# Performance work log

Measured on AMD Instinct MI355X. Metric: run time of the kernel, lower is better.

## Reference

```python
import jax, jax.numpy as jnp
import numpy as np

N = 10000      # atoms
F = 32         # nr_atom_basis
H = 7          # nr_heads
C = F * H      # nr_coefficients = 224
E = 200000     # edges
NRBF = 50
CUTOFF = 5.0
EPS = 1e-8


def _seg_sum(x, idx, n):
    return jax.ops.segment_sum(x, idx, num_segments=n)


def _seg_mean(x, idx, n):
    # torch scatter_reduce 'mean' with include_self=False: sum/count, 0 for empty segments
    s = _seg_sum(x, idx, n)
    cnt = _seg_sum(jnp.ones((x.shape[0],), x.dtype), idx, n)
    cnt = jnp.maximum(cnt, 1.0).reshape((n,) + (1,) * (x.ndim - 1))
    return s / cnt


def _scatter_softmax(w, idx, n):
    m = jax.ops.segment_max(w, idx, num_segments=n)
    m = jnp.where(jnp.isfinite(m), m, 0.0)  # guard empty segments
    e = jnp.exp(w - m[idx])
    s = _seg_sum(e, idx, n)
    return e / s[idx]


def setup_inputs():
    key = jax.random.key(0)
    ks = jax.random.split(key, 16)
    def w(k, shape, scale=0.1):
        return jax.random.normal(k, shape, jnp.float32) * scale
    return {
        "h": w(ks[0], (N, F), 1.0),
        "x": w(ks[1], (N, 3), 1.0),
        "v": w(ks[2], (N, 3), 0.1),
        "pairlist": jax.random.randint(ks[3], (2, E), 0, N),
        "w_in": w(ks[4], (2 * F, NRBF)), "b_in": jnp.zeros((NRBF,), jnp.float32),
        "w_e1": w(ks[5], (2 * F + NRBF + 1, F)), "b_e1": jnp.zeros((F,), jnp.float32),
        "w_e2": w(ks[6], (F, F)), "b_e2": jnp.zeros((F,), jnp.float32),
        "w_att": w(ks[7], (F, H)), "b_att": jnp.zeros((H,), jnp.float32),
        "w_n1": w(ks[8], (F + C + F, F)), "b_n1": jnp.zeros((F,), jnp.float32),
        "w_n2": w(ks[9], (F, F)), "b_n2": jnp.zeros((F,), jnp.float32),
        "w_pn1": w(ks[10], (C, F)), "b_pn1": jnp.zeros((F,), jnp.float32),
        "w_pn2": w(ks[11], (F, F)), "b_pn2": jnp.zeros((F,), jnp.float32),
        "w_v1": w(ks[12], (F, F)), "b_v1": jnp.zeros((F,), jnp.float32),
        "w_v2": w(ks[13], (F, 1)),
        "w_xmix": w(ks[14], (C, C)),
        "w_vmix": w(ks[15], (C, 1)),
    }


def reference(h, x, v, pairlist, w_in, b_in, w_e1, b_e1, w_e2, b_e2,
              w_att, b_att, w_n1, b_n1, w_n2, b_n2, w_pn1, b_pn1,
              w_pn2, b_pn2, w_v1, b_v1, w_v2, w_xmix, w_vmix):
    act = jax.nn.silu
    idx_i, idx_j = pairlist[0], pairlist[1]
    n = h.shape[0]

    r_ij = x[idx_j] - x[idx_i]                      # [E,3]
    d_ij = jnp.linalg.norm(r_ij, axis=-1)           # [E]
    dir_ij = r_ij / (d_ij[:, None] + EPS)           # [E,3]

    # edge model: continuous-filter conv with concatenation
    h_cat = jnp.concatenate([h[idx_i], h[idx_j]], axis=-1)           # [E,2F]
    centers = jnp.linspace(0.0, CUTOFF, NRBF)
    width = centers[1] - centers[0]
    rbf = jnp.exp(-0.5 * ((d_ij[:, None] - centers) / width) ** 2)   # [E,NRBF]
    filt = rbf * (h_cat @ w_in + b_in)                               # [E,NRBF]
    edge_in = jnp.concatenate([h_cat, filt, d_ij[:, None]], axis=-1)
    h_ij_edge = act(edge_in @ w_e1 + b_e1) @ w_e2 + b_e2             # [E,F]

    # semantic attention (scatter softmax over edges grouped by idx_i)
    att_w = jax.nn.celu(h_ij_edge @ w_att + b_att, alpha=2.0)        # [E,H]
    cut = 0.5 * (jnp.cos(jnp.pi * d_ij / CUTOFF) + 1.0) * (d_ij < CUTOFF)
    att = _scatter_softmax(att_w * cut[:, None], idx_i, n)           # [E,H]
    # einsum('pf,ph->pfh').reshape -> f-major, h-minor
    h_ij_sem = (h_ij_edge[:, :, None] * att[:, None, :]).reshape(-1, C)  # [E,C]
    h_i_sem = _seg_sum(h_ij_sem, idx_i, n)                           # [N,C]

    # equivariant combinations + spatial attention
    comb = jnp.tanh(h_ij_sem @ w_xmix)[:, :, None] * dir_ij[:, None, :]  # [E,C,3]
    comb_mean = _seg_mean(comb, idx_i, n)                            # [N,C,3]
    cnsq = jnp.sum(comb_mean ** 2, axis=-1)                          # [N,C]
    h_i_spatial = act(act(cnsq @ w_pn1 + b_pn1) @ w_pn2 + b_pn2)     # [N,F]

    # node update
    node_in = jnp.concatenate([h, h_i_sem, h_i_spatial], axis=-1)
    h_upd = h + act(act(node_in @ w_n1 + b_n1) @ w_n2 + b_n2)        # [N,F]

    # velocity update
    v_ij = jnp.einsum('ecx,c->ex', comb, w_vmix[:, 0])               # [E,3]
    dv = _seg_mean(v_ij, idx_i, n)                                   # [N,3]
    gate = 2.0 * jax.nn.sigmoid(act(h @ w_v1 + b_v1) @ w_v2)         # [N,1]
    v_upd = gate * v + dv
    x_upd = x + v_upd
    return h_upd, x_upd, v_upd
```

## Files before the change

kernel.cpp:

```cpp
#include <hip/hip_runtime.h>
#include <hip/hip_bf16.h>
#include <math.h>

typedef unsigned short u16;
typedef __attribute__((ext_vector_type(8))) short bf16x8;
typedef __attribute__((ext_vector_type(4))) float f32x4;

constexpr int kF    = 32;
constexpr int kH    = 7;
constexpr int kC    = 224;
constexpr int kRBF  = 50;
constexpr int kM    = 128;
constexpr int kStr  = 232;
constexpr int kEM   = 128;
constexpr int kAStr = 136;
constexpr int kBStr = 40;
constexpr float kCut = 5.0f;
constexpr float kEps = 1e-8f;

__device__ __forceinline__ float silu_f(float a) { return a / (1.f + __expf(-a)); }
__device__ __forceinline__ float tanh_f(float x) {
    float e = __expf(2.f * x);
    return 1.f - 2.f / (e + 1.f);
}
__device__ __forceinline__ float bf2f(u16 u) {
    union { unsigned int i; float f; } v; v.i = ((unsigned int)u) << 16; return v.f;
}
__device__ __forceinline__ u16 f2bf(float f) {
    union { float f; unsigned int i; } v; v.f = f;
    unsigned int x = v.i;
    unsigned int round = ((x >> 16) & 1u) + 0x7fffu;
    return (u16)((x + round) >> 16);
}
__device__ __forceinline__ unsigned pk2(float a, float b) {
    union { __hip_bfloat162 h; unsigned u; } v;
    v.h = __float22bfloat162_rn(make_float2(a, b));
    return v.u;
}

__global__ __launch_bounds__(256) void init_kernel(
    const float* __restrict__ wx, const float* __restrict__ w_in,
    const float* __restrict__ w_e1, const float* __restrict__ w_e2,
    const float* __restrict__ w_att, const float* __restrict__ b_e2,
    const float* __restrict__ b_att, const int* __restrict__ pl,
    u16* __restrict__ wxT, u16* __restrict__ W1T, u16* __restrict__ W2T,
    u16* __restrict__ W3T, u16* __restrict__ W24T, float* __restrict__ b24,
    int* __restrict__ counts, int E_)
{
    int idx = blockIdx.x * 256 + threadIdx.x;
    if (idx < kC * kC) {
        int c = idx / kC, k = idx - c * kC;
        wxT[idx] = f2bf(wx[k * kC + c]);
    }
    for (int e = idx; e < E_; e += gridDim.x * 256) atomicAdd(&counts[pl[e]], 1);

    if (blockIdx.x == 0) {
        int t = threadIdx.x;
        for (int i = t; i < 64 * 64; i += 256) {
            int n = i >> 6, k = i & 63;
            W1T[i] = f2bf((n < kRBF) ? w_in[k * kRBF + n] : 0.f);
        }
        for (int i = t; i < 32 * 128; i += 256) {
            int n = i >> 7, k = i & 127;
            W2T[i] = f2bf((k < 115) ? w_e1[k * kF + n] : 0.f);
        }
        for (int i = t; i < 32 * 32; i += 256) {
            int n = i >> 5, k = i & 31;
            W3T[i] = f2bf(w_e2[k * kF + n]);
        }
        for (int i = t; i < 16 * 32; i += 256) {
            int n = i >> 5, k = i & 31;
            float a = 0.f;
            if (n < kH) for (int o = 0; o < kF; o++) a += w_e2[k * kF + o] * w_att[o * kH + n];
            W24T[i] = f2bf(a);
        }
        if (t < kH) {
            float a = b_att[t];
            for (int o = 0; o < kF; o++) a += b_e2[o] * w_att[o * kH + t];
            b24[t] = a;
        }
    }
}

__global__ __launch_bounds__(1024) void scan_kernel(
    const int* __restrict__ counts, int* __restrict__ offsets, int n)
{
    __shared__ int buf[1024];
    int t = threadIdx.x;
    int chunk = (n + 1023) >> 10;
    int lo = t * chunk;
    int s = 0;
    for (int i = 0; i < chunk; i++) {
        int g = lo + i;
        if (g < n) s += counts[g];
    }
    buf[t] = s;
    __syncthreads();
    for (int off = 1; off < 1024; off <<= 1) {
        int v = (t >= off) ? buf[t - off] : 0;
        __syncthreads();
        buf[t] += v;
        __syncthreads();
    }
    int run = buf[t] - s;
    for (int i = 0; i < chunk; i++) {
        int g = lo + i;
        if (g < n) { offsets[g] = run; run += counts[g]; }
    }
    if (t == 1023) offsets[n] = buf[1023];
}

__global__ __launch_bounds__(256) void scatter_kernel(
    const int* __restrict__ pl, const int* __restrict__ offsets,
    int* __restrict__ cursor, int* __restrict__ rank, int* __restrict__ nid, int E_)
{
    int e = blockIdx.x * 256 + threadIdx.x;
    if (e < E_) {
        int i = pl[e];
        int p = atomicAdd(&cursor[i], 1);
        int pos = offsets[i] + p;
        rank[e] = pos;
        nid[pos] = i;
    }
}

__global__ __launch_bounds__(256) void edge_kernel(
    const float* __restrict__ h, const float* __restrict__ x,
    const int* __restrict__ pl, const int* __restrict__ rank_g, int E_,
    const float* __restrict__ b_in, const float* __restrict__ b_e1,
    const float* __restrict__ b_e2,
    const u16* __restrict__ W1T, const u16* __restrict__ W2T,
    const u16* __restrict__ W3T, const u16* __restrict__ W24T,
    const float* __restrict__ b24,
    float* __restrict__ he_g, float* __restrict__ logit_g,
    float* __restrict__ dir_g)
{
    __shared__ __align__(16) u16 s_A[kEM][kAStr];
    __shared__ __align__(16) u16 s_t1[kEM][kBStr];
    __shared__ float s_d[kEM];
    __shared__ int   s_r[kEM];

    int t = threadIdx.x;
    int T0 = blockIdx.x * kEM;
    int w = t >> 6, lane = t & 63, quad = lane >> 4, l15 = lane & 15;

    {
        int e = t >> 1, half = t & 1;
        int ge = T0 + e;
        bool val = ge < E_;
        int i = 0, j = 0;
        if (val) { i = pl[ge]; j = pl[E_ + ge]; }
        const float4* pi = (const float4*)(h + (size_t)i * kF) + half * 4;
        const float4* pj = (const float4*)(h + (size_t)j * kF) + half * 4;
#pragma unroll
        for (int q = 0; q < 4; q++) {
            float4 a = val ? pi[q] : make_float4(0.f, 0.f, 0.f, 0.f);
            float4 b = val ? pj[q] : make_float4(0.f, 0.f, 0.f, 0.f);
            unsigned* di = (unsigned*)&s_A[e][half * 16 + 4 * q];
            di[0] = pk2(a.x, a.y); di[1] = pk2(a.z, a.w);
            unsigned* dj = (unsigned*)&s_A[e][kF + half * 16 + 4 * q];
            dj[0] = pk2(b.x, b.y); dj[1] = pk2(b.z, b.w);
        }
        if (half == 0) {
            float d = 0.f;
            int r = 0;
            if (val) {
                r = rank_g[ge];
                float r0 = x[j * 3 + 0] - x[i * 3 + 0];
                float r1 = x[j * 3 + 1] - x[i * 3 + 1];
                float r2 = x[j * 3 + 2] - x[i * 3 + 2];
                d = sqrtf(r0 * r0 + r1 * r1 + r2 * r2);
                float inv = 1.0f / (d + kEps);
                dir_g[(size_t)r * 3 + 0] = r0 * inv;
                dir_g[(size_t)r * 3 + 1] = r1 * inv;
                dir_g[(size_t)r * 3 + 2] = r2 * inv;
            }
            s_r[e] = r;
            s_d[e] = d;
            s_A[e][114] = f2bf(d);
            s_A[e][115] = 0;
            unsigned* z = (unsigned*)&s_A[e][116];
#pragma unroll
            for (int q = 0; q < 6; q++) z[q] = 0u;
        }
    }
    __syncthreads();

    const float invw = 49.0f / kCut;

    {
        bf16x8 a1[2][2];
#pragma unroll
        for (int rt = 0; rt < 2; rt++)
#pragma unroll
            for (int kt = 0; kt < 2; kt++)
                a1[rt][kt] = *(const bf16x8*)&s_A[32 * w + 16 * rt + l15][kt * 32 + quad * 8];
#pragma unroll
        for (int ct = 0; ct < 4; ct++) {
            int c = ct * 16 + l15;
            bf16x8 b0 = *(const bf16x8*)(W1T + (size_t)c * 64 + quad * 8);
            bf16x8 b1 = *(const bf16x8*)(W1T + (size_t)c * 64 + 32 + quad * 8);
            float bin = (c < kRBF) ? b_in[c] : 0.f;
#pragma unroll
            for (int rt = 0; rt < 2; rt++) {
                f32x4 acc = {0.f, 0.f, 0.f, 0.f};
                acc = __builtin_amdgcn_mfma_f32_16x16x32_bf16(a1[rt][0], b0, acc, 0, 0, 0);
                acc = __builtin_amdgcn_mfma_f32_16x16x32_bf16(a1[rt][1], b1, acc, 0, 0, 0);
                if (c < kRBF) {
#pragma unroll
                    for (int r = 0; r < 4; r++) {
                        int row = 32 * w + 16 * rt + quad * 4 + r;
                        float arg = s_d[row] * invw - (float)c;
                        float filt = __expf(-0.5f * arg * arg) * (acc[r] + bin);
                        s_A[row][64 + c] = f2bf(filt);
                    }
                }
            }
        }
    }

    {
        bf16x8 a2[2][4];
#pragma unroll
        for (int rt = 0; rt < 2; rt++)
#pragma unroll
            for (int kt = 0; kt < 4; kt++)
                a2[rt][kt] = *(const bf16x8*)&s_A[32 * w + 16 * rt + l15][kt * 32 + quad * 8];
#pragma unroll
        for (int ct = 0; ct < 2; ct++) {
            int c = ct * 16 + l15;
            bf16x8 bb[4];
#pragma unroll
            for (int kt = 0; kt < 4; kt++)
                bb[kt] = *(const bf16x8*)(W2T + (size_t)c * 128 + kt * 32 + quad * 8);
            float be = b_e1[c];
#pragma unroll
            for (int rt = 0; rt < 2; rt++) {
                f32x4 acc = {0.f, 0.f, 0.f, 0.f};
#pragma unroll
                for (int kt = 0; kt < 4; kt++)
                    acc = __builtin_amdgcn_mfma_f32_16x16x32_bf16(a2[rt][kt], bb[kt], acc, 0, 0, 0);
#pragma unroll
                for (int r = 0; r < 4; r++) {
                    int row = 32 * w + 16 * rt + quad * 4 + r;
                    s_t1[row][c] = f2bf(silu_f(acc[r] + be));
                }
            }
        }
    }

    {
        bf16x8 a3[2];
#pragma unroll
        for (int rt = 0; rt < 2; rt++)
            a3[rt] = *(const bf16x8*)&s_t1[32 * w + 16 * rt + l15][quad * 8];

#pragma unroll
        for (int ct = 0; ct < 2; ct++) {
            int c = ct * 16 + l15;
            bf16x8 b3 = *(const bf16x8*)(W3T + (size_t)c * 32 + quad * 8);
            float be = b_e2[c];
#pragma unroll
            for (int rt = 0; rt < 2; rt++) {
                f32x4 acc = {0.f, 0.f, 0.f, 0.f};
                acc = __builtin_amdgcn_mfma_f32_16x16x32_bf16(a3[rt], b3, acc, 0, 0, 0);
#pragma unroll
                for (int r = 0; r < 4; r++) {
                    int row = 32 * w + 16 * rt + quad * 4 + r;
                    int ge = T0 + row;
                    if (ge < E_) he_g[(size_t)s_r[row] * kF + c] = acc[r] + be;
                }
            }
        }
        {
            bf16x8 b4 = *(const bf16x8*)(W24T + (size_t)l15 * 32 + quad * 8);
            float bb = (l15 < kH) ? b24[l15] : 0.f;
#pragma unroll
            for (int rt = 0; rt < 2; rt++) {
                f32x4 acc = {0.f, 0.f, 0.f, 0.f};
                acc = __builtin_amdgcn_mfma_f32_16x16x32_bf16(a3[rt], b4, acc, 0, 0, 0);
                if (l15 < kH) {
#pragma unroll
                    for (int r = 0; r < 4; r++) {
                        int row = 32 * w + 16 * rt + quad * 4 + r;
                        int ge = T0 + row;
                        if (ge < E_) {
                            float a = acc[r] + bb;
                            a = (a >= 0.f) ? a : 2.f * (__expf(0.5f * a) - 1.f);
                            float dd = s_d[row];
                            float cut = (dd < kCut)
                                ? 0.5f * (__cosf(0.62831853071795864f * dd) + 1.f) : 0.f;
                            logit_g[(size_t)s_r[row] * kH + l15] = a * cut;
                        }
                    }
                }
            }
        }
    }
}

__global__ __launch_bounds__(256) void stats_kernel(
    const float* __restrict__ logit_g, const int* __restrict__ offsets,
    float* __restrict__ m_g, float* __restrict__ invs_g, int N_)
{
    int wave = threadIdx.x >> 6;
    int lane = threadIdx.x & 63;
    int node = blockIdx.x * 4 + wave;
    if (node >= N_) return;
    int base = offsets[node];
    int deg  = offsets[node + 1] - base;

    float m[kH], ss[kH];
#pragma unroll
    for (int hh = 0; hh < kH; hh++) { m[hh] = -1e30f; ss[hh] = 0.f; }
    for (int e = lane; e < deg; e += 64) {
        const float* lp = logit_g + (size_t)(base + e) * kH;
#pragma unroll
        for (int hh = 0; hh < kH; hh++) {
            float vv = lp[hh];
            if (vv > m[hh]) { ss[hh] *= __expf(m[hh] - vv); m[hh] = vv; }
            ss[hh] += __expf(vv - m[hh]);
        }
    }
#pragma unroll
    for (int hh = 0; hh < kH; hh++) {
        float mm = m[hh], s2 = ss[hh];
#pragma unroll
        for (int off = 32; off >= 1; off >>= 1) {
            float mo = __shfl_xor(mm, off);
            float so = __shfl_xor(s2, off);
            float mn = fmaxf(mm, mo);
            s2 = s2 * __expf(mm - mn) + so * __expf(mo - mn);
            mm = mn;
        }
        if (lane == 0) {
            m_g[(size_t)node * kH + hh] = mm;
            invs_g[(size_t)node * kH + hh] = (s2 > 0.f) ? 1.f / s2 : 0.f;
        }
    }
}

__global__ __launch_bounds__(256) void xmix_kernel(
    const float* __restrict__ he_g, const float* __restrict__ logit_g,
    const float* __restrict__ dir_g, const int* __restrict__ nid,
    const float* __restrict__ m_g, const float* __restrict__ invs_g,
    const u16* __restrict__ wxT, int E_,
    float* __restrict__ nodeacc, float* __restrict__ bpart, int* __restrict__ bid)
{
    __shared__ __align__(16) u16 s_buf[kM][kStr];
    __shared__ float s_att[kM][kH];
    __shared__ __align__(16) float s_dir4[kM][4];
    __shared__ int   s_node[kM];
    __shared__ int   s_prev, s_next;

    int t = threadIdx.x;
    int T0 = blockIdx.x * kM;
    int cp = min(kM, E_ - T0);

    if (t < kM) s_node[t] = (T0 + t < E_) ? nid[T0 + t] : -1;
    if (t == 0) {
        s_prev = (T0 > 0) ? nid[T0 - 1] : -2;
        s_next = (T0 + cp < E_) ? nid[T0 + cp] : -2;
    }
    __syncthreads();

    int w    = t >> 6;
    int lane = t & 63;
    int quad = lane >> 4;
    int l15  = lane & 15;

    int ws = 32 * w;
    int we = min(ws + 32, cp);
    bool winvalid = (ws < cp);
    bool contL = false, contR = false;
    if (winvalid) {
        int nfirst = s_node[ws], nlast = s_node[we - 1];
        contL = (w == 0) ? (s_prev == nfirst) : (s_node[ws - 1] == nfirst);
        contR = (we == cp) ? (s_next == nlast) : (s_node[we] == nlast);
    }
    if (lane == 0) {
        int b0 = -1, b1 = -1;
        if (winvalid) {
            int nfirst = s_node[ws], nlast = s_node[we - 1];
            b0 = contL ? nfirst : -1;
            if (contR && !(nfirst == nlast && contL)) b1 = nlast;
        }
        bid[8 * blockIdx.x + 2 * w + 0] = b0;
        bid[8 * blockIdx.x + 2 * w + 1] = b1;
    }
    bool active_w = winvalid && (lane < 56);
    int c0 = 4 * lane;

    for (int idx = t; idx < kM * kH; idx += 256) {
        int e = idx / kH, hh = idx - e * kH;
        float a = 0.f;
        if (T0 + e < E_) {
            int nd = s_node[e];
            a = __expf(logit_g[(size_t)(T0 + e) * kH + hh] - m_g[(size_t)nd * kH + hh])
                * invs_g[(size_t)nd * kH + hh];
        }
        s_att[e][hh] = a;
    }
    for (int idx = t; idx < cp * 3; idx += 256) {
        int e = idx / 3, xx = idx - e * 3;
        s_dir4[e][xx] = dir_g[(size_t)(T0 + e) * 3 + xx];
    }
    __syncthreads();

#pragma unroll
    for (int p = 0; p < kM * kF / 256; p++) {
        int idx = t + 256 * p;
        int e = idx >> 5, f = idx & 31;
        float hv = (T0 + e < E_) ? he_g[(size_t)(T0 + e) * kF + f] : 0.f;
        float sv[7];
#pragma unroll
        for (int hh = 0; hh < kH; hh++) sv[hh] = hv * s_att[e][hh];
        u16* dst = &s_buf[e][f * 7];
        if ((f & 1) == 0) {
            *(unsigned*)(dst)     = pk2(sv[0], sv[1]);
            *(unsigned*)(dst + 2) = pk2(sv[2], sv[3]);
            *(unsigned*)(dst + 4) = pk2(sv[4], sv[5]);
            dst[6] = f2bf(sv[6]);
        } else {
            dst[0] = f2bf(sv[0]);
            *(unsigned*)(dst + 1) = pk2(sv[1], sv[2]);
            *(unsigned*)(dst + 3) = pk2(sv[3], sv[4]);
            *(unsigned*)(dst + 5) = pk2(sv[5], sv[6]);
        }
    }
    __syncthreads();

    if (active_w) {
        float hs0 = 0.f, hs1 = 0.f, hs2 = 0.f, hs3 = 0.f;
        int rs = ws;
        for (int e = ws; e < we; e++) {
            if (s_node[e] != s_node[rs]) {
                bool comp = (rs > ws) || !contL;
                float4 vv = make_float4(hs0, hs1, hs2, hs3);
                if (comp) *(float4*)&nodeacc[(size_t)s_node[rs] * 896 + 672 + c0] = vv;
                else *(float4*)&bpart[(size_t)(8 * blockIdx.x + 2 * w) * 896 + 672 + c0] = vv;
                hs0 = hs1 = hs2 = hs3 = 0.f; rs = e;
            }
            uint2 pv = *(const uint2*)&s_buf[e][c0];
            hs0 += bf2f((u16)pv.x); hs1 += bf2f((u16)(pv.x >> 16));
            hs2 += bf2f((u16)pv.y); hs3 += bf2f((u16)(pv.y >> 16));
        }
        bool t0 = (rs == ws);
        bool comp = ((!t0) || !contL) && !contR;
        float4 vv = make_float4(hs0, hs1, hs2, hs3);
        if (comp) *(float4*)&nodeacc[(size_t)s_node[rs] * 896 + 672 + c0] = vv;
        else {
            int slot = (t0 && contL) ? 0 : 1;
            *(float4*)&bpart[(size_t)(8 * blockIdx.x + 2 * w + slot) * 896 + 672 + c0] = vv;
        }
    }

    bf16x8 afr[2][7];
#pragma unroll
    for (int rt = 0; rt < 2; rt++)
#pragma unroll
        for (int kt = 0; kt < 7; kt++)
            afr[rt][kt] = *(const bf16x8*)&s_buf[32 * w + 16 * rt + l15][kt * 32 + quad * 8];

    bf16x8 bb[3][7];
#pragma unroll
    for (int kt = 0; kt < 7; kt++)
        bb[0][kt] = *(const bf16x8*)(wxT + (size_t)l15 * kC + kt * 32 + quad * 8);
#pragma unroll
    for (int kt = 0; kt < 7; kt++)
        bb[1][kt] = *(const bf16x8*)(wxT + (size_t)(16 + l15) * kC + kt * 32 + quad * 8);
    __syncthreads();

#pragma unroll
    for (int ct = 0; ct < 14; ct++) {
        const int cur = ct % 3;
        const int nxt = (ct + 2) % 3;
        if (ct < 12) {
            const u16* bp = wxT + (size_t)((ct + 2) * 16 + l15) * kC + quad * 8;
#pragma unroll
            for (int kt = 0; kt < 7; kt++) bb[nxt][kt] = *(const bf16x8*)(bp + kt * 32);
        }
        f32x4 acc0 = {0.f, 0.f, 0.f, 0.f};
        f32x4 acc1 = {0.f, 0.f, 0.f, 0.f};
#pragma unroll
        for (int kt = 0; kt < 7; kt++) {
            acc0 = __builtin_amdgcn_mfma_f32_16x16x32_bf16(afr[0][kt], bb[cur][kt], acc0, 0, 0, 0);
            acc1 = __builtin_amdgcn_mfma_f32_16x16x32_bf16(afr[1][kt], bb[cur][kt], acc1, 0, 0, 0);
        }
        int colg = ct * 16 + l15;
#pragma unroll
        for (int s = 0; s < 2; s++) {
            f32x4 ac = s ? acc1 : acc0;
            int rbase = 32 * w + 16 * s + quad * 4;
            unsigned p01 = pk2(tanh_f(ac[0]), tanh_f(ac[1]));
            unsigned p23 = pk2(tanh_f(ac[2]), tanh_f(ac[3]));
            s_buf[rbase + 0][colg] = (u16)p01;
            s_buf[rbase + 1][colg] = (u16)(p01 >> 16);
            s_buf[rbase + 2][colg] = (u16)p23;
            s_buf[rbase + 3][colg] = (u16)(p23 >> 16);
        }
    }
    __syncthreads();

    if (active_w) {
        float a0[4] = {0.f, 0.f, 0.f, 0.f};
        float a1[4] = {0.f, 0.f, 0.f, 0.f};
        float a2[4] = {0.f, 0.f, 0.f, 0.f};
        int rs = ws;
        for (int e = ws; e < we; e++) {
            if (s_node[e] != s_node[rs]) {
                bool comp = (rs > ws) || !contL;
                float* p = comp ? (nodeacc + (size_t)s_node[rs] * 896)
                                : (bpart + (size_t)(8 * blockIdx.x + 2 * w) * 896);
                *(float4*)&p[c0]       = make_float4(a0[0], a0[1], a0[2], a0[3]);
                *(float4*)&p[224 + c0] = make_float4(a1[0], a1[1], a1[2], a1[3]);
                *(float4*)&p[448 + c0] = make_float4(a2[0], a2[1], a2[2], a2[3]);
#pragma unroll
                for (int q = 0; q < 4; q++) { a0[q] = 0.f; a1[q] = 0.f; a2[q] = 0.f; }
                rs = e;
            }
            float4 dd = *(const float4*)&s_dir4[e][0];
            uint2 pv = *(const uint2*)&s_buf[e][c0];
            float Tv[4];
            Tv[0] = bf2f((u16)pv.x); Tv[1] = bf2f((u16)(pv.x >> 16));
            Tv[2] = bf2f((u16)pv.y); Tv[3] = bf2f((u16)(pv.y >> 16));
#pragma unroll
            for (int q = 0; q < 4; q++) {
                a0[q] += Tv[q] * dd.x;
                a1[q] += Tv[q] * dd.y;
                a2[q] += Tv[q] * dd.z;
            }
        }
        bool t0 = (rs == ws);
        bool comp = ((!t0) || !contL) && !contR;
        float* p;
        if (comp) p = nodeacc + (size_t)s_node[rs] * 896;
        else {
            int slot = (t0 && contL) ? 0 : 1;
            p = bpart + (size_t)(8 * blockIdx.x + 2 * w + slot) * 896;
        }
        *(float4*)&p[c0]       = make_float4(a0[0], a0[1], a0[2], a0[3]);
        *(float4*)&p[224 + c0] = make_float4(a1[0], a1[1], a1[2], a1[3]);
        *(float4*)&p[448 + c0] = make_float4(a2[0], a2[1], a2[2], a2[3]);
    }
}

__global__ __launch_bounds__(256) void node_kernel(
    const float* __restrict__ h, const float* __restrict__ x, const float* __restrict__ v,
    const float* __restrict__ nodeacc, const float* __restrict__ bpart,
    const int* __restrict__ bid, const int* __restrict__ offs,
    const float* __restrict__ w_n1, const float* __restrict__ b_n1,
    const float* __restrict__ w_n2, const float* __restrict__ b_n2,
    const float* __restrict__ w_pn1, const float* __restrict__ b_pn1,
    const float* __restrict__ w_pn2, const float* __restrict__ b_pn2,
    const float* __restrict__ w_v1, const float* __restrict__ b_v1,
    const float* __restrict__ w_v2, const float* __restrict__ w_vmix,
    float* __restrict__ out_h, float* __restrict__ out_x, float* __restrict__ out_v,
    int N_)
{
    __shared__ float s_cm[4][3][kC];
    __shared__ float s_cnsq[4][kC];
    __shared__ float s_ni[4][288];
    __shared__ float s_part[8][4][kF];
    __shared__ float s_hn[4][kF], s_sp1[4][kF], s_spat[4][kF], s_n1v[4][kF], s_g1[4][kF];
    __shared__ float s_pdv[4][3][8];
    __shared__ float s_gate[4], s_dv[4][3];

    int t = threadIdx.x;
    int n0 = blockIdx.x * 4;

    if (t < kC) {
        for (int nd = 0; nd < 4; nd++) {
            int node = n0 + nd;
            if (node >= N_) break;
            int base = offs[node], end = offs[node + 1];
            int deg = end - base;
            float a0 = 0.f, a1 = 0.f, a2 = 0.f, hh = 0.f;
            if (deg > 0) {
                int wlo = base >> 5, whi = (end - 1) >> 5;
                if (wlo == whi) {
                    const float* p = nodeacc + (size_t)node * 896;
                    a0 = p[t]; a1 = p[224 + t]; a2 = p[448 + t]; hh = p[672 + t];
                } else {
                    for (int W = wlo; W <= whi; W++) {
#pragma unroll
                        for (int s = 0; s < 2; s++) {
                            if (bid[2 * W + s] == node) {
                                const float* p = bpart + (size_t)(2 * W + s) * 896;
                                a0 += p[t]; a1 += p[224 + t]; a2 += p[448 + t]; hh += p[672 + t];
                            }
                        }
                    }
                }
            }
            float invc = 1.f / fmaxf((float)deg, 1.f);
            float m0 = a0 * invc, m1 = a1 * invc, m2 = a2 * invc;
            s_cm[nd][0][t] = m0; s_cm[nd][1][t] = m1; s_cm[nd][2][t] = m2;
            s_cnsq[nd][t] = m0 * m0 + m1 * m1 + m2 * m2;
            s_ni[nd][kF + t] = hh;
        }
    } else {
        int ln = t - 224;
        for (int nd = 0; nd < 4; nd++) {
            int node = n0 + nd;
            float hv = (node < N_) ? h[(size_t)node * kF + ln] : 0.f;
            s_hn[nd][ln] = hv;
            s_ni[nd][ln] = hv;
        }
    }
    __syncthreads();

    int o = t & 31, g = t >> 5;
    {
        float acc[4] = {0.f, 0.f, 0.f, 0.f};
        int cb = g * 28;
        for (int i = 0; i < 28; i++) {
            float wv = w_pn1[(cb + i) * kF + o];
#pragma unroll
            for (int nd = 0; nd < 4; nd++) acc[nd] += s_cnsq[nd][cb + i] * wv;
        }
#pragma unroll
        for (int nd = 0; nd < 4; nd++) s_part[g][nd][o] = acc[nd];
    }
    __syncthreads();
    if (t < 128) {
        int nd = t >> 5;
        float a = b_pn1[o];
#pragma unroll
        for (int g2 = 0; g2 < 8; g2++) a += s_part[g2][nd][o];
        s_sp1[nd][o] = silu_f(a);
    } else {
        int nd = (t - 128) >> 5;
        float a = b_v1[o];
        for (int f = 0; f < kF; f++) a += s_hn[nd][f] * w_v1[f * kF + o];
        s_g1[nd][o] = silu_f(a);
    }
    __syncthreads();
    if (t < 128) {
        int nd = t >> 5;
        float a = b_pn2[o];
        for (int o2 = 0; o2 < kF; o2++) a += s_sp1[nd][o2] * w_pn2[o2 * kF + o];
        s_spat[nd][o] = silu_f(a);
    } else if (t < 132) {
        int nd = t - 128;
        float a = 0.f;
        for (int o2 = 0; o2 < kF; o2++) a += s_g1[nd][o2] * w_v2[o2];
        s_gate[nd] = 2.f / (1.f + __expf(-a));
    } else if (t >= 160) {
        int q = t - 160; int nd = q / 24; int r = q - nd * 24;
        int xx = r >> 3, ln = r & 7;
        float a = 0.f;
        for (int c = ln; c < kC; c += 8) a += w_vmix[c] * s_cm[nd][xx][c];
        s_pdv[nd][xx][ln] = a;
    }
    __syncthreads();
    if (t < 128) {
        int nd = t >> 5;
        s_ni[nd][kF + kC + o] = s_spat[nd][o];
    } else if (t < 140) {
        int q = t - 128; int nd = q / 3; int xx = q - nd * 3;
        float a = 0.f;
#pragma unroll
        for (int ln = 0; ln < 8; ln++) a += s_pdv[nd][xx][ln];
        s_dv[nd][xx] = a;
    }
    __syncthreads();
    {
        float acc[4] = {0.f, 0.f, 0.f, 0.f};
        int rb = g * 36;
        for (int i = 0; i < 36; i++) {
            float wv = w_n1[(rb + i) * kF + o];
#pragma unroll
            for (int nd = 0; nd < 4; nd++) acc[nd] += s_ni[nd][rb + i] * wv;
        }
#pragma unroll
        for (int nd = 0; nd < 4; nd++) s_part[g][nd][o] = acc[nd];
    }
    __syncthreads();
    if (t < 128) {
        int nd = t >> 5;
        float a = b_n1[o];
#pragma unroll
        for (int g2 = 0; g2 < 8; g2++) a += s_part[g2][nd][o];
        s_n1v[nd][o] = silu_f(a);
    }
    __syncthreads();
    if (t < 128) {
        int nd = t >> 5; int node = n0 + nd;
        if (node < N_) {
            float a = b_n2[o];
            for (int o2 = 0; o2 < kF; o2++) a += s_n1v[nd][o2] * w_n2[o2 * kF + o];
            out_h[(size_t)node * kF + o] = s_hn[nd][o] + silu_f(a);
        }
    } else if (t < 140) {
        int q = t - 128; int nd = q / 3; int xx = q - nd * 3;
        int node = n0 + nd;
        if (node < N_) {
            float vv = v[(size_t)node * 3 + xx];
            float vu = s_gate[nd] * vv + s_dv[nd][xx];
            out_v[(size_t)node * 3 + xx] = vu;
            out_x[(size_t)node * 3 + xx] = x[(size_t)node * 3 + xx] + vu;
        }
    }
}

extern "C" void kernel_launch(void* const* d_in, const int* in_sizes, int n_in,
                              void* d_out, int out_size, void* d_ws, size_t ws_size,
                              hipStream_t stream)
{
    const float* h      = (const float*)d_in[0];
    const float* x      = (const float*)d_in[1];
    const float* v      = (const float*)d_in[2];
    const int*   pl     = (const int*)d_in[3];
    const float* w_in   = (const float*)d_in[4];
    const float* b_in   = (const float*)d_in[5];
    const float* w_e1   = (const float*)d_in[6];
    const float* b_e1   = (const float*)d_in[7];
    const float* w_e2   = (const float*)d_in[8];
    const float* b_e2   = (const float*)d_in[9];
    const float* w_att  = (const float*)d_in[10];
    const float* b_att  = (const float*)d_in[11];
    const float* w_n1   = (const float*)d_in[12];
    const float* b_n1   = (const float*)d_in[13];
    const float* w_n2   = (const float*)d_in[14];
    const float* b_n2   = (const float*)d_in[15];
    const float* w_pn1  = (const float*)d_in[16];
    const float* b_pn1  = (const float*)d_in[17];
    const float* w_pn2  = (const float*)d_in[18];
    const float* b_pn2  = (const float*)d_in[19];
    const float* w_v1   = (const float*)d_in[20];
    const float* b_v1   = (const float*)d_in[21];
    const float* w_v2   = (const float*)d_in[22];
    const float* w_xmix = (const float*)d_in[23];
    const float* w_vmix = (const float*)d_in[24];

    const int E_ = in_sizes[3] / 2;
    const int N_ = in_sizes[0] / kF;
    const int nblk = (E_ + kM - 1) / kM;

    char* w = (char*)d_ws;
    u16*   wxT     = (u16*)w;   w += (size_t)kC * kC * 2;
    u16*   W1T     = (u16*)w;   w += (size_t)64 * 64 * 2;
    u16*   W2T     = (u16*)w;   w += (size_t)32 * 128 * 2;
    u16*   W3T     = (u16*)w;   w += (size_t)32 * 32 * 2;
    u16*   W24T    = (u16*)w;   w += (size_t)16 * 32 * 2;
    float* b24     = (float*)w; w += 8 * 4;
    float* he_g    = (float*)w; w += (size_t)E_ * kF * 4;
    float* logit_g = (float*)w; w += (size_t)E_ * kH * 4;
    float* dir_g   = (float*)w; w += (size_t)E_ * 3 * 4;
    float* m_g     = (float*)w; w += (size_t)N_ * kH * 4;
    float* invs_g  = (float*)w; w += (size_t)N_ * kH * 4;
    float* nodeacc = (float*)w; w += (size_t)N_ * 896 * 4;
    float* bpart   = (float*)w; w += (size_t)8 * nblk * 896 * 4;
    int*   bid     = (int*)w;   w += (size_t)8 * nblk * 4;
    int* counts    = (int*)w;   w += (size_t)N_ * 4;
    int* offs      = (int*)w;   w += (size_t)(N_ + 1) * 4;
    int* cursor    = (int*)w;   w += (size_t)N_ * 4;
    int* rank_g    = (int*)w;   w += (size_t)E_ * 4;
    int* nid       = (int*)w;   w += (size_t)E_ * 4;

    float* out_h = (float*)d_out;
    float* out_x = out_h + (size_t)N_ * kF;
    float* out_v = out_x + (size_t)N_ * 3;

    hipMemsetAsync(counts, 0, (size_t)N_ * 4, stream);
    hipMemsetAsync(cursor, 0, (size_t)N_ * 4, stream);

    init_kernel<<<dim3((kC * kC + 255) / 256), dim3(256), 0, stream>>>(
        w_xmix, w_in, w_e1, w_e2, w_att, b_e2, b_att, pl,
        wxT, W1T, W2T, W3T, W24T, b24, counts, E_);

    scan_kernel<<<dim3(1), dim3(1024), 0, stream>>>(counts, offs, N_);

    scatter_kernel<<<dim3((E_ + 255) / 256), dim3(256), 0, stream>>>(
        pl, offs, cursor, rank_g, nid, E_);

    edge_kernel<<<dim3((E_ + kEM - 1) / kEM), dim3(256), 0, stream>>>(
        h, x, pl, rank_g, E_, b_in, b_e1, b_e2, W1T, W2T, W3T, W24T, b24,
        he_g, logit_g, dir_g);

    stats_kernel<<<dim3((N_ + 3) / 4), dim3(256), 0, stream>>>(
        logit_g, offs, m_g, invs_g, N_);

    xmix_kernel<<<dim3(nblk), dim3(256), 0, stream>>>(
        he_g, logit_g, dir_g, nid, m_g, invs_g, wxT, E_,
        nodeacc, bpart, bid);

    node_kernel<<<dim3((N_ + 3) / 4), dim3(256), 0, stream>>>(
        h, x, v, nodeacc, bpart, bid, offs,
        w_n1, b_n1, w_n2, b_n2, w_pn1, b_pn1, w_pn2, b_pn2,
        w_v1, b_v1, w_v2, w_vmix, out_h, out_x, out_v, N_);
}
```

Measured before the change: 348.4 us.

## Fuse scatter into edge kernel, store edge features as bf16, retune stats and prefetch

Drops the separate scatter kernel: the edge kernel now claims each edge's CSR slot with an atomic on the cursor and writes nid itself, which removes one launch and the rank array round trip. Per-edge hidden features are stored as bf16 rather than fp32, halving that intermediate's traffic at some precision cost. The stats kernel moves from one 64-lane wave per node to a 32-lane group per node, since degrees are around 20. The xmix weight prefetch goes from 3 to 4 buffers, which raises register pressure.

```diff
diff --git a/kernel.cpp b/kernel.cpp
--- a/kernel.cpp
+++ b/kernel.cpp
@@ -110,29 +110,16 @@
     if (t == 1023) offsets[n] = buf[1023];
 }
 
-__global__ __launch_bounds__(256) void scatter_kernel(
-    const int* __restrict__ pl, const int* __restrict__ offsets,
-    int* __restrict__ cursor, int* __restrict__ rank, int* __restrict__ nid, int E_)
-{
-    int e = blockIdx.x * 256 + threadIdx.x;
-    if (e < E_) {
-        int i = pl[e];
-        int p = atomicAdd(&cursor[i], 1);
-        int pos = offsets[i] + p;
-        rank[e] = pos;
-        nid[pos] = i;
-    }
-}
-
 __global__ __launch_bounds__(256) void edge_kernel(
     const float* __restrict__ h, const float* __restrict__ x,
-    const int* __restrict__ pl, const int* __restrict__ rank_g, int E_,
+    const int* __restrict__ pl, const int* __restrict__ offs,
+    int* __restrict__ cursor, int* __restrict__ nid, int E_,
     const float* __restrict__ b_in, const float* __restrict__ b_e1,
     const float* __restrict__ b_e2,
     const u16* __restrict__ W1T, const u16* __restrict__ W2T,
     const u16* __restrict__ W3T, const u16* __restrict__ W24T,
     const float* __restrict__ b24,
-    float* __restrict__ he_g, float* __restrict__ logit_g,
+    u16* __restrict__ he_g, float* __restrict__ logit_g,
     float* __restrict__ dir_g)
 {
     __shared__ __align__(16) u16 s_A[kEM][kAStr];
@@ -165,7 +152,9 @@
             float d = 0.f;
             int r = 0;
             if (val) {
-                r = rank_g[ge];
+                int p = atomicAdd(&cursor[i], 1);
+                r = offs[i] + p;
+                nid[r] = i;
                 float r0 = x[j * 3 + 0] - x[i * 3 + 0];
                 float r1 = x[j * 3 + 1] - x[i * 3 + 1];
                 float r2 = x[j * 3 + 2] - x[i * 3 + 2];
@@ -268,7 +257,7 @@
                 for (int r = 0; r < 4; r++) {
                     int row = 32 * w + 16 * rt + quad * 4 + r;
                     int ge = T0 + row;
-                    if (ge < E_) he_g[(size_t)s_r[row] * kF + c] = acc[r] + be;
+                    if (ge < E_) he_g[(size_t)s_r[row] * kF + c] = f2bf(acc[r] + be);
                 }
             }
         }
@@ -303,9 +292,9 @@
     const float* __restrict__ logit_g, const int* __restrict__ offsets,
     float* __restrict__ m_g, float* __restrict__ invs_g, int N_)
 {
-    int wave = threadIdx.x >> 6;
-    int lane = threadIdx.x & 63;
-    int node = blockIdx.x * 4 + wave;
+    int grp  = threadIdx.x >> 5;
+    int lane = threadIdx.x & 31;
+    int node = blockIdx.x * 8 + grp;
     if (node >= N_) return;
     int base = offsets[node];
     int deg  = offsets[node + 1] - base;
@@ -313,7 +302,7 @@
     float m[kH], ss[kH];
 #pragma unroll
     for (int hh = 0; hh < kH; hh++) { m[hh] = -1e30f; ss[hh] = 0.f; }
-    for (int e = lane; e < deg; e += 64) {
+    for (int e = lane; e < deg; e += 32) {
         const float* lp = logit_g + (size_t)(base + e) * kH;
 #pragma unroll
         for (int hh = 0; hh < kH; hh++) {
@@ -326,7 +315,7 @@
     for (int hh = 0; hh < kH; hh++) {
         float mm = m[hh], s2 = ss[hh];
 #pragma unroll
-        for (int off = 32; off >= 1; off >>= 1) {
+        for (int off = 16; off >= 1; off >>= 1) {
             float mo = __shfl_xor(mm, off);
             float so = __shfl_xor(s2, off);
             float mn = fmaxf(mm, mo);
@@ -341,7 +330,7 @@
 }
 
 __global__ __launch_bounds__(256) void xmix_kernel(
-    const float* __restrict__ he_g, const float* __restrict__ logit_g,
+    const u16* __restrict__ he_g, const float* __restrict__ logit_g,
     const float* __restrict__ dir_g, const int* __restrict__ nid,
     const float* __restrict__ m_g, const float* __restrict__ invs_g,
     const u16* __restrict__ wxT, int E_,
@@ -411,7 +400,7 @@
     for (int p = 0; p < kM * kF / 256; p++) {
         int idx = t + 256 * p;
         int e = idx >> 5, f = idx & 31;
-        float hv = (T0 + e < E_) ? he_g[(size_t)(T0 + e) * kF + f] : 0.f;
+        float hv = (T0 + e < E_) ? bf2f(he_g[(size_t)(T0 + e) * kF + f]) : 0.f;
         float sv[7];
 #pragma unroll
         for (int hh = 0; hh < kH; hh++) sv[hh] = hv * s_att[e][hh];
@@ -462,21 +451,20 @@
         for (int kt = 0; kt < 7; kt++)
             afr[rt][kt] = *(const bf16x8*)&s_buf[32 * w + 16 * rt + l15][kt * 32 + quad * 8];
 
-    bf16x8 bb[3][7];
-#pragma unroll
-    for (int kt = 0; kt < 7; kt++)
-        bb[0][kt] = *(const bf16x8*)(wxT + (size_t)l15 * kC + kt * 32 + quad * 8);
-#pragma unroll
-    for (int kt = 0; kt < 7; kt++)
-        bb[1][kt] = *(const bf16x8*)(wxT + (size_t)(16 + l15) * kC + kt * 32 + quad * 8);
+    bf16x8 bb[4][7];
+#pragma unroll
+    for (int b = 0; b < 3; b++)
+#pragma unroll
+        for (int kt = 0; kt < 7; kt++)
+            bb[b][kt] = *(const bf16x8*)(wxT + (size_t)(16 * b + l15) * kC + kt * 32 + quad * 8);
     __syncthreads();
 
 #pragma unroll
     for (int ct = 0; ct < 14; ct++) {
-        const int cur = ct % 3;
-        const int nxt = (ct + 2) % 3;
-        if (ct < 12) {
-            const u16* bp = wxT + (size_t)((ct + 2) * 16 + l15) * kC + quad * 8;
+        const int cur = ct & 3;
+        const int nxt = (ct + 3) & 3;
+        if (ct < 11) {
+            const u16* bp = wxT + (size_t)((ct + 3) * 16 + l15) * kC + quad * 8;
 #pragma unroll
             for (int kt = 0; kt < 7; kt++) bb[nxt][kt] = *(const bf16x8*)(bp + kt * 32);
         }
@@ -745,7 +733,7 @@
     u16*   W3T     = (u16*)w;   w += (size_t)32 * 32 * 2;
     u16*   W24T    = (u16*)w;   w += (size_t)16 * 32 * 2;
     float* b24     = (float*)w; w += 8 * 4;
-    float* he_g    = (float*)w; w += (size_t)E_ * kF * 4;
+    u16*   he_g    = (u16*)w;   w += (size_t)E_ * kF * 2;
     float* logit_g = (float*)w; w += (size_t)E_ * kH * 4;
     float* dir_g   = (float*)w; w += (size_t)E_ * 3 * 4;
     float* m_g     = (float*)w; w += (size_t)N_ * kH * 4;
@@ -756,7 +744,6 @@
     int* counts    = (int*)w;   w += (size_t)N_ * 4;
     int* offs      = (int*)w;   w += (size_t)(N_ + 1) * 4;
     int* cursor    = (int*)w;   w += (size_t)N_ * 4;
-    int* rank_g    = (int*)w;   w += (size_t)E_ * 4;
     int* nid       = (int*)w;   w += (size_t)E_ * 4;
 
     float* out_h = (float*)d_out;
@@ -772,14 +759,11 @@
 
     scan_kernel<<<dim3(1), dim3(1024), 0, stream>>>(counts, offs, N_);
 
-    scatter_kernel<<<dim3((E_ + 255) / 256), dim3(256), 0, stream>>>(
-        pl, offs, cursor, rank_g, nid, E_);
-
     edge_kernel<<<dim3((E_ + kEM - 1) / kEM), dim3(256), 0, stream>>>(
-        h, x, pl, rank_g, E_, b_in, b_e1, b_e2, W1T, W2T, W3T, W24T, b24,
-        he_g, logit_g, dir_g);
-
-    stats_kernel<<<dim3((N_ + 3) / 4), dim3(256), 0, stream>>>(
+        h, x, pl, offs, cursor, nid, E_, b_in, b_e1, b_e2,
+        W1T, W2T, W3T, W24T, b24, he_g, logit_g, dir_g);
+
+    stats_kernel<<<dim3((N_ + 7) / 8), dim3(256), 0, stream>>>(
         logit_g, offs, m_g, invs_g, N_);
 
     xmix_kernel<<<dim3(nblk), dim3(256), 0, stream>>>(
```

After: 334.7 us. 3.9% less time.
